# Kernel tuning notes

Hardware: AMD Instinct MI355X
Metric: run time of the kernel (lower is better)

Reference implementation:

```python
import jax, jax.numpy as jnp
import numpy as np

B, T, FEAT, IN = 32, 96, 2048, 4096  # batch, frames, feature_len, inshape (cat mode)


def setup_inputs() -> dict:
    key = jax.random.key(0)
    ks = jax.random.split(key, 12)
    s = 1.0 / np.sqrt(FEAT)  # PyTorch LSTMCell/Linear init scale ~ U(-1/sqrt(hidden), ...)
    f32 = jnp.float32
    return {
        "feature": jax.random.normal(ks[0], (B, T, IN), f32),
        "gumbel_u": jax.random.uniform(ks[1], (T - 1, B, 2), f32),
        "W_ih": jax.random.normal(ks[2], (4 * FEAT, IN), f32) * s,
        "b_ih": jax.random.normal(ks[3], (4 * FEAT,), f32) * s,
        "W_hh": jax.random.normal(ks[4], (4 * FEAT, FEAT), f32) * s,
        "b_hh": jax.random.normal(ks[5], (4 * FEAT,), f32) * s,
        "W_pred": jax.random.normal(ks[6], (2, FEAT), f32) * s,
        "b_pred": jax.random.normal(ks[7], (2,), f32) * s,
        "W_util": jax.random.normal(ks[8], (1, FEAT), f32) * s,
        "b_util": jax.random.normal(ks[9], (1,), f32) * s,
        "W_use": jax.random.normal(ks[10], (2, FEAT), f32) * s,
        "b_use": jax.random.normal(ks[11], (2,), f32) * s,
    }


def reference(feature, gumbel_u, W_ih, b_ih, W_hh, b_hh,
              W_pred, b_pred, W_util, b_util, W_use, b_use):
    tau = 1.0
    eps = 1e-10
    x = jnp.transpose(feature, (1, 0, 2))          # [T, B, IN]
    gnoise = -jnp.log(-jnp.log(gumbel_u + eps) + eps)  # Gumbel(0,1), [T-1, B, 2]

    def lstm_cell(x_t, h, c):
        gates = x_t @ W_ih.T + b_ih + h @ W_hh.T + b_hh  # [B, 4F]
        i, f, g, o = jnp.split(gates, 4, axis=-1)        # PyTorch gate order i,f,g,o
        c2 = jax.nn.sigmoid(f) * c + jax.nn.sigmoid(i) * jnp.tanh(g)
        h2 = jax.nn.sigmoid(o) * jnp.tanh(c2)
        return h2, c2

    def heads(h):
        return h @ W_pred.T + b_pred, h @ W_util.T + b_util

    h0 = jnp.zeros((x.shape[1], FEAT), x.dtype)
    h, c = lstm_cell(x[0], h0, h0)                   # step 0: no gating
    pred0, util0 = heads(h)

    def step(carry, inp):
        h_prev, c_prev = carry
        x_t, g_t = inp
        h_new, c2 = lstm_cell(x_t, h_prev, c_prev)
        logits = h_new @ W_use.T + b_use             # [B, 2]
        use = jax.nn.softmax((logits + g_t) / tau, axis=-1)  # soft gumbel-softmax
        # bmm(stack([h_prev, h_new], -1), use) == convex mix of the two states
        h2 = h_prev * use[:, :1] + h_new * use[:, 1:2]
        pred, util = heads(h2)
        return (h2, c2), (pred, util)

    _, (preds, utils) = jax.lax.scan(step, (h, c), (x[1:], gnoise))
    pred = jnp.concatenate([pred0[None], preds], axis=0)   # [T, B, 2]
    util = jnp.concatenate([util0[None], utils], axis=0)   # [T, B, 1]
    return pred, util
```

## Files before the change

kernel.cpp:

```cpp
#include <hip/hip_runtime.h>
#include <cstdint>
#include <cstddef>

#define TT 96
#define BB 32
#define FEATD 2048
#define IND 4096
#define NG 8192
#define MROWS 3072

typedef _Float16 half8 __attribute__((ext_vector_type(8)));
typedef _Float16 half4 __attribute__((ext_vector_type(4)));
typedef _Float16 half2v __attribute__((ext_vector_type(2)));
typedef float f32x4 __attribute__((ext_vector_type(4)));

#define WS_FEAT16 0u
#define WS_HBUF   0u
#define WS_WIH16  25165824u
#define WS_WHH16  92274688u
#define WS_PRE16  125829120u
#define WS_GAB    176160768u
#define WS_HD     176185344u
#define WS_BAR    176222208u

#define NWG 256
#define BAR_WORDS 8192

__global__ void __launch_bounds__(256) k_convert(
    const float* __restrict__ feat, const float* __restrict__ wih,
    const float* __restrict__ whh,
    _Float16* __restrict__ feat16, _Float16* __restrict__ wih16,
    _Float16* __restrict__ whh16, unsigned* __restrict__ flags)
{
  size_t id = (size_t)blockIdx.x * blockDim.x + threadIdx.x;
  size_t stride = (size_t)gridDim.x * blockDim.x;
  for (size_t i = id; i < (size_t)MROWS * IND / 4; i += stride) {
    f32x4 v = ((const f32x4*)feat)[i];
    half4 h = { (_Float16)v[0], (_Float16)v[1], (_Float16)v[2], (_Float16)v[3] };
    ((half4*)feat16)[i] = h;
  }
  for (size_t i = id; i < (size_t)NG * IND / 4; i += stride) {
    f32x4 v = ((const f32x4*)wih)[i];
    half4 h = { (_Float16)v[0], (_Float16)v[1], (_Float16)v[2], (_Float16)v[3] };
    ((half4*)wih16)[i] = h;
  }
  for (size_t i = id; i < (size_t)NG * FEATD / 4; i += stride) {
    f32x4 v = ((const f32x4*)whh)[i];
    half4 h = { (_Float16)v[0], (_Float16)v[1], (_Float16)v[2], (_Float16)v[3] };
    ((half4*)whh16)[i] = h;
  }
  for (size_t i = id; i < BAR_WORDS; i += stride) flags[i] = 0u;
}

__device__ __forceinline__ void gload16(const _Float16* g, _Float16* l) {
  __builtin_amdgcn_global_load_lds(
      (const __attribute__((address_space(1))) void*)g,
      (__attribute__((address_space(3))) void*)l, 16, 0, 0);
}

__global__ void __launch_bounds__(256, 1) k_gemm(
    const _Float16* __restrict__ A,
    const _Float16* __restrict__ Bw,
    const float* __restrict__ bih, const float* __restrict__ bhh,
    _Float16* __restrict__ C)
{
  __shared__ __align__(16) _Float16 As[128 * 32];
  __shared__ __align__(16) _Float16 Bs[128 * 32];
  const int tid = threadIdx.x;
  const int lane = tid & 63;
  const int wave = tid >> 6;
  const int wm = wave >> 1, wn = wave & 1;
  const int mbase = blockIdx.y * 128;
  const int nbase = blockIdx.x * 128;

  f32x4 acc[4][4] = {};
  const int r0 = lane >> 2;
  const int kc = (lane & 3) * 8;
  const int rr = lane & 15;
  const int ko = (lane >> 4) * 8;

  for (int k0 = 0; k0 < IND; k0 += 32) {
    for (int i = 0; i < 2; ++i) {
      int seg = wave * 2 + i;
      int row = seg * 16 + r0;
      gload16(A + (size_t)(mbase + row) * IND + k0 + kc, As + seg * 512);
      gload16(Bw + (size_t)(nbase + row) * IND + k0 + kc, Bs + seg * 512);
    }
    __syncthreads();
    half8 af[4], bf[4];
    for (int f = 0; f < 4; ++f) {
      af[f] = *(const half8*)(As + (wm * 64 + f * 16 + rr) * 32 + ko);
      bf[f] = *(const half8*)(Bs + (wn * 64 + f * 16 + rr) * 32 + ko);
    }
    for (int fm = 0; fm < 4; ++fm)
      for (int fn = 0; fn < 4; ++fn)
        acc[fm][fn] = __builtin_amdgcn_mfma_f32_16x16x32_f16(af[fm], bf[fn], acc[fm][fn], 0, 0, 0);
    __syncthreads();
  }
  for (int fn = 0; fn < 4; ++fn) {
    int n = nbase + wn * 64 + fn * 16 + (lane & 15);
    float bias = bih[n] + bhh[n];
    for (int fm = 0; fm < 4; ++fm) {
      int m0 = mbase + wm * 64 + fm * 16 + (lane >> 4) * 4;
      for (int r = 0; r < 4; ++r)
        C[(size_t)(m0 + r) * NG + n] = (_Float16)(acc[fm][fn][r] + bias);
    }
  }
}

#define LDS_WHH 0
#define LDS_RED 131072
#define RED_STRIDE_F 1152
#define LDS_TOTAL 149504

__device__ __forceinline__ float fast_sigmoid(float x) {
  return 1.f / (1.f + __expf(-x));
}
__device__ __forceinline__ float fast_tanh(float x) {
  return 1.f - 2.f / (__expf(2.f * x) + 1.f);
}

__global__ void __launch_bounds__(512, 1) k_recur(
    const float* __restrict__ gumbel,
    const float* __restrict__ Wuse, const float* __restrict__ buse,
    const _Float16* __restrict__ whh16,
    const _Float16* __restrict__ pre16,
    _Float16* __restrict__ hbuf,
    float* __restrict__ gab,
    unsigned* __restrict__ flags)
{
  extern __shared__ __align__(16) char smem[];
  const int tid = threadIdx.x;
  const int wg = blockIdx.x;
  const int wave = tid >> 6, lane = tid & 63;
  float* RED = (float*)(smem + LDS_RED);

  {
    int c = tid >> 4;
    int grow = (c >> 3) * FEATD + wg * 8 + (c & 7);
    const _Float16* src = whh16 + (size_t)grow * FEATD;
    char* dst = smem + LDS_WHH + c * 4096;
    int x = c & 7;
    for (int i = 0; i < 16; ++i) {
      int g = (tid & 15) + i * 16;
      *(half8*)(dst + ((g ^ x) << 4)) = *(const half8*)(src + g * 8);
    }
  }

  const int rr = lane & 15;
  const int lk = (lane >> 4) * 8;
  half8 uq0[8], uq1[8];
#pragma unroll
  for (int s = 0; s < 8; ++s) {
    int kk = wave * 256 + s * 32 + lk;
#pragma unroll
    for (int e = 0; e < 8; ++e) {
      uq0[s][e] = (_Float16)Wuse[kk + e];
      uq1[s][e] = (_Float16)Wuse[FEATD + kk + e];
    }
  }

  const int b_ = tid >> 3, fi_ = tid & 7;
  const float bq0 = buse[0], bq1 = buse[1];

  float G0 = 0.f, G1 = 0.f, G2 = 0.f, G3 = 0.f, cc = 0.f;
  const _Float16* prbase = pre16 + ((size_t)b_ * TT) * NG + wg * 8 + fi_;
  _Float16 pf0 = 0, pf1 = 0, pf2 = 0, pf3 = 0;
  _Float16 pn0 = 0, pn1 = 0, pn2 = 0, pn3 = 0;
  float gmc0 = 0.f, gmc1 = 0.f, gmn0 = 0.f, gmn1 = 0.f;
  if (tid < 256) {
    pf0 = prbase[0]; pf1 = prbase[FEATD]; pf2 = prbase[2 * FEATD]; pf3 = prbase[3 * FEATD];
  }
  __syncthreads();

  for (int t = 0; t < TT; ++t) {
    if (tid < 256 && t + 1 < TT) {
      const _Float16* p = prbase + (size_t)(t + 1) * NG;
      pn0 = p[0]; pn1 = p[FEATD]; pn2 = p[2 * FEATD]; pn3 = p[3 * FEATD];
      gmn0 = gumbel[(size_t)t * 64 + b_ * 2 + 0];
      gmn1 = gumbel[(size_t)t * 64 + b_ * 2 + 1];
    }
    if (tid < 256) {
      float ig = fast_sigmoid((float)pf0 + G0);
      float fg = fast_sigmoid((float)pf1 + G1);
      float gg = fast_tanh((float)pf2 + G2);
      float og = fast_sigmoid((float)pf3 + G3);
      cc = fg * cc + ig * gg;
      float hn = og * fast_tanh(cc);
      float hn_o = __shfl_xor(hn, 1);
      if ((fi_ & 1) == 0) {
        union { _Float16 h[2]; unsigned u; } pk;
        pk.h[0] = (_Float16)hn; pk.h[1] = (_Float16)hn_o;
        unsigned* dst = (unsigned*)(hbuf + (size_t)t * (BB * FEATD) + b_ * FEATD + wg * 8 + fi_);
        __hip_atomic_store(dst, pk.u, __ATOMIC_RELAXED, __HIP_MEMORY_SCOPE_AGENT);
      }
    }
    __syncthreads();
    const unsigned tgt = (unsigned)(t + 1);
    if (tid == 0)
      __hip_atomic_store(&flags[wg * 16], tgt, __ATOMIC_RELAXED, __HIP_MEMORY_SCOPE_AGENT);
    if (wg == 0) {
      if (wave == 0) {
        for (;;) {
          bool ok = true;
#pragma unroll
          for (int j = 0; j < 4; ++j) {
            unsigned v = __hip_atomic_load(&flags[(lane * 4 + j) * 16],
                                           __ATOMIC_RELAXED, __HIP_MEMORY_SCOPE_AGENT);
            ok &= (v >= tgt);
          }
          if (__all(ok)) break;
          __builtin_amdgcn_s_sleep(1);
        }
#pragma unroll
        for (int j = 0; j < 4; ++j)
          __hip_atomic_store(&flags[4096 + (lane * 4 + j) * 16], tgt,
                             __ATOMIC_RELAXED, __HIP_MEMORY_SCOPE_AGENT);
      }
    } else {
      if (tid == 0) {
        while (__hip_atomic_load(&flags[4096 + wg * 16],
                                 __ATOMIC_RELAXED, __HIP_MEMORY_SCOPE_AGENT) < tgt)
          __builtin_amdgcn_s_sleep(1);
      }
    }
    __syncthreads();

    const _Float16* hb = hbuf + (size_t)t * (BB * FEATD);
    f32x4 acc[2][2] = {};
    float q0a = 0.f, q1a = 0.f, q0b = 0.f, q1b = 0.f;
    {
      const int c0 = rr, c1 = 16 + rr;
      const char* wsl = smem + LDS_WHH;
#pragma unroll
      for (int s = 0; s < 8; ++s) {
        int kk = wave * 256 + s * 32 + lk;
        half8 a0 = *(const half8*)(hb + rr * FEATD + kk);
        half8 a1 = *(const half8*)(hb + (16 + rr) * FEATD + kk);
        int g = kk >> 3;
        half8 b0 = *(const half8*)(wsl + c0 * 4096 + ((g ^ (c0 & 7)) << 4));
        half8 b1 = *(const half8*)(wsl + c1 * 4096 + ((g ^ (c1 & 7)) << 4));
        acc[0][0] = __builtin_amdgcn_mfma_f32_16x16x32_f16(a0, b0, acc[0][0], 0, 0, 0);
        acc[0][1] = __builtin_amdgcn_mfma_f32_16x16x32_f16(a0, b1, acc[0][1], 0, 0, 0);
        acc[1][0] = __builtin_amdgcn_mfma_f32_16x16x32_f16(a1, b0, acc[1][0], 0, 0, 0);
        acc[1][1] = __builtin_amdgcn_mfma_f32_16x16x32_f16(a1, b1, acc[1][1], 0, 0, 0);
        const half2v* a0p = (const half2v*)&a0;
        const half2v* a1p = (const half2v*)&a1;
        const half2v* u0p = (const half2v*)&uq0[s];
        const half2v* u1p = (const half2v*)&uq1[s];
#pragma unroll
        for (int e = 0; e < 4; ++e) {
          q0a = __builtin_amdgcn_fdot2(a0p[e], u0p[e], q0a, false);
          q1a = __builtin_amdgcn_fdot2(a0p[e], u1p[e], q1a, false);
          q0b = __builtin_amdgcn_fdot2(a1p[e], u0p[e], q0b, false);
          q1b = __builtin_amdgcn_fdot2(a1p[e], u1p[e], q1b, false);
        }
      }
    }
    q0a += __shfl_xor(q0a, 16); q0a += __shfl_xor(q0a, 32);
    q1a += __shfl_xor(q1a, 16); q1a += __shfl_xor(q1a, 32);
    q0b += __shfl_xor(q0b, 16); q0b += __shfl_xor(q0b, 32);
    q1b += __shfl_xor(q1b, 16); q1b += __shfl_xor(q1b, 32);
    if (lane < 16) {
      float* pads = RED + (wave & 3) * RED_STRIDE_F + 32 + (wave >> 2) * 2;
      pads[rr * 36 + 0] = q0a; pads[rr * 36 + 1] = q1a;
      pads[(16 + rr) * 36 + 0] = q0b; pads[(16 + rr) * 36 + 1] = q1b;
    }
    {
      const int bb0 = (lane >> 4) * 4;
      const int cc0 = lane & 15;
      if (wave >= 4) {
        float* s0 = RED + (wave - 4) * RED_STRIDE_F;
        for (int fm = 0; fm < 2; ++fm)
          for (int fn = 0; fn < 2; ++fn)
            *(f32x4*)(s0 + (fn * 16 + cc0) * 36 + fm * 16 + bb0) = acc[fm][fn];
      }
      __syncthreads();
      if (wave < 4) {
        float* s0 = RED + wave * RED_STRIDE_F;
        for (int fm = 0; fm < 2; ++fm)
          for (int fn = 0; fn < 2; ++fn) {
            acc[fm][fn] += *(f32x4*)(s0 + (fn * 16 + cc0) * 36 + fm * 16 + bb0);
            *(f32x4*)(s0 + (fn * 16 + cc0) * 36 + fm * 16 + bb0) = acc[fm][fn];
          }
      }
      __syncthreads();
    }
    if (tid < 256) {
      float ga = 0.f, gb = 1.f;
      if (t > 0) {
        float q0 = bq0, q1 = bq1;
#pragma unroll
        for (int s2 = 0; s2 < 4; ++s2) {
          const float* pp = RED + s2 * RED_STRIDE_F + b_ * 36 + 32;
          q0 += pp[0] + pp[2]; q1 += pp[1] + pp[3];
        }
        float n0 = -logf(-logf(gmc0 + 1e-10f) + 1e-10f);
        float n1 = -logf(-logf(gmc1 + 1e-10f) + 1e-10f);
        float l0 = q0 + n0;
        float l1 = q1 + n1;
        float mx = fmaxf(l0, l1);
        float e0 = __expf(l0 - mx), e1 = __expf(l1 - mx);
        float inv = 1.f / (e0 + e1);
        ga = e0 * inv; gb = e1 * inv;
        if (wg == 0 && fi_ == 0) {
          gab[(t * BB + b_) * 2 + 0] = ga;
          gab[(t * BB + b_) * 2 + 1] = gb;
        }
      }
      {
        const int base = fi_ * 36 + b_;
        float m0 = RED[base] + RED[RED_STRIDE_F + base] + RED[2 * RED_STRIDE_F + base] + RED[3 * RED_STRIDE_F + base];
        float m1 = RED[base + 8 * 36] + RED[RED_STRIDE_F + base + 8 * 36] + RED[2 * RED_STRIDE_F + base + 8 * 36] + RED[3 * RED_STRIDE_F + base + 8 * 36];
        float m2 = RED[base + 16 * 36] + RED[RED_STRIDE_F + base + 16 * 36] + RED[2 * RED_STRIDE_F + base + 16 * 36] + RED[3 * RED_STRIDE_F + base + 16 * 36];
        float m3 = RED[base + 24 * 36] + RED[RED_STRIDE_F + base + 24 * 36] + RED[2 * RED_STRIDE_F + base + 24 * 36] + RED[3 * RED_STRIDE_F + base + 24 * 36];
        G0 = ga * G0 + gb * m0;
        G1 = ga * G1 + gb * m1;
        G2 = ga * G2 + gb * m2;
        G3 = ga * G3 + gb * m3;
      }
      pf0 = pn0; pf1 = pn1; pf2 = pn2; pf3 = pn3;
      gmc0 = gmn0; gmc1 = gmn1;
    }
  }
}

__global__ void __launch_bounds__(256) k_heads(
    const _Float16* __restrict__ hbuf,
    const float* __restrict__ Wpred, const float* __restrict__ Wutil,
    float* __restrict__ hd)
{
  const int t = blockIdx.x;
  const int tid = threadIdx.x;
  const int b = tid >> 3, fi = tid & 7;
  const _Float16* h = hbuf + ((size_t)t * BB + b) * FEATD;
  float d0 = 0.f, d1 = 0.f, d2 = 0.f;
  for (int j = 0; j < 32; ++j) {
    int k = fi * 8 + j * 64;
    half8 v = *(const half8*)(h + k);
#pragma unroll
    for (int e = 0; e < 8; ++e) {
      float x = (float)v[e];
      d0 += x * Wpred[k + e];
      d1 += x * Wpred[FEATD + k + e];
      d2 += x * Wutil[k + e];
    }
  }
  for (int m = 1; m < 8; m <<= 1) {
    d0 += __shfl_xor(d0, m); d1 += __shfl_xor(d1, m); d2 += __shfl_xor(d2, m);
  }
  if (fi == 0) {
    float* o = hd + ((size_t)t * BB + b) * 3;
    o[0] = d0; o[1] = d1; o[2] = d2;
  }
}

__global__ void __launch_bounds__(64) k_scan(
    const float* __restrict__ hd,
    const float* __restrict__ gab,
    const float* __restrict__ bpred, const float* __restrict__ butil,
    float* __restrict__ out)
{
  const int b = threadIdx.x;
  if (b >= BB) return;
  const float bp0 = bpred[0], bp1 = bpred[1], bu0 = butil[0];
  float L0 = hd[b * 3 + 0], L1 = hd[b * 3 + 1], L2 = hd[b * 3 + 2];
  out[b * 2 + 0] = L0 + bp0;
  out[b * 2 + 1] = L1 + bp1;
  out[TT * BB * 2 + b] = L2 + bu0;
  for (int t = 1; t < TT; ++t) {
    float ga = gab[(t * BB + b) * 2 + 0];
    float gb = gab[(t * BB + b) * 2 + 1];
    const float* d = hd + ((size_t)t * BB + b) * 3;
    L0 = ga * L0 + gb * d[0];
    L1 = ga * L1 + gb * d[1];
    L2 = ga * L2 + gb * d[2];
    out[(t * BB + b) * 2 + 0] = L0 + bp0;
    out[(t * BB + b) * 2 + 1] = L1 + bp1;
    out[TT * BB * 2 + t * BB + b] = L2 + bu0;
  }
}

extern "C" void kernel_launch(void* const* d_in, const int* in_sizes, int n_in,
                              void* d_out, int out_size, void* d_ws, size_t ws_size,
                              hipStream_t stream) {
  const float* feat  = (const float*)d_in[0];
  const float* gumb  = (const float*)d_in[1];
  const float* Wih   = (const float*)d_in[2];
  const float* bih   = (const float*)d_in[3];
  const float* Whh   = (const float*)d_in[4];
  const float* bhh   = (const float*)d_in[5];
  const float* Wpred = (const float*)d_in[6];
  const float* bpred = (const float*)d_in[7];
  const float* Wutil = (const float*)d_in[8];
  const float* butil = (const float*)d_in[9];
  const float* Wuse  = (const float*)d_in[10];
  const float* buse  = (const float*)d_in[11];

  char* ws = (char*)d_ws;
  _Float16* feat16 = (_Float16*)(ws + WS_FEAT16);
  _Float16* hbufp  = (_Float16*)(ws + WS_HBUF);
  _Float16* wih16  = (_Float16*)(ws + WS_WIH16);
  _Float16* whh16  = (_Float16*)(ws + WS_WHH16);
  _Float16* pre16  = (_Float16*)(ws + WS_PRE16);
  float*    gabp   = (float*)(ws + WS_GAB);
  float*    hdp    = (float*)(ws + WS_HD);
  unsigned* flagp  = (unsigned*)(ws + WS_BAR);

  (void)in_sizes; (void)n_in; (void)out_size; (void)ws_size;

  hipFuncSetAttribute((const void*)k_recur,
                      hipFuncAttributeMaxDynamicSharedMemorySize, LDS_TOTAL);

  k_convert<<<2048, 256, 0, stream>>>(feat, Wih, Whh, feat16, wih16, whh16, flagp);
  dim3 g2(NG / 128, MROWS / 128);
  k_gemm<<<g2, 256, 0, stream>>>(feat16, wih16, bih, bhh, pre16);
  k_recur<<<NWG, 512, LDS_TOTAL, stream>>>(gumb, Wuse, buse, whh16, pre16,
                                           hbufp, gabp, flagp);
  k_heads<<<TT, 256, 0, stream>>>(hbufp, Wpred, Wutil, hdp);
  k_scan<<<1, 64, 0, stream>>>(hdp, gabp, bpred, butil, (float*)d_out);
}
```

Baseline: 1.044 ms.

## Split batch into two half-groups and ping-pong recurrence phases across grid barriers

The 32-batch recurrence is split into two independent 16-row halves (A and B) with separate flag sets and LDS reduction buffers. While one half waits on its grid-wide barrier, the other half's h·W_hh matmul and gate update run, so barrier latency overlaps with compute. This adds extra barriers, more per-step phases, and more complex flag and gumbel index bookkeeping that must stay correct.

```diff
diff --git a/kernel.cpp b/kernel.cpp
--- a/kernel.cpp
+++ b/kernel.cpp
@@ -24,7 +24,11 @@
 #define WS_BAR    176222208u
 
 #define NWG 256
-#define BAR_WORDS 8192
+#define BAR_WORDS 16384
+#define AR_A 0
+#define AR_B 4096
+#define RL_A 8192
+#define RL_B 12288
 
 __global__ void __launch_bounds__(256) k_convert(
     const float* __restrict__ feat, const float* __restrict__ wih,
@@ -109,15 +113,87 @@
 }
 
 #define LDS_WHH 0
-#define LDS_RED 131072
-#define RED_STRIDE_F 1152
-#define LDS_TOTAL 149504
+#define SLOT_F 640
+#define LDS_REDA 131072
+#define LDS_REDB 141312
+#define LDS_TOTAL 151552
 
 __device__ __forceinline__ float fast_sigmoid(float x) {
   return 1.f / (1.f + __expf(-x));
 }
 __device__ __forceinline__ float fast_tanh(float x) {
   return 1.f - 2.f / (__expf(2.f * x) + 1.f);
+}
+
+__device__ __forceinline__ void agg_release(unsigned* flags, int arBase, int rlBase,
+                                            unsigned tgt, int lane) {
+  for (;;) {
+    bool ok = true;
+#pragma unroll
+    for (int j = 0; j < 4; ++j) {
+      unsigned v = __hip_atomic_load(&flags[arBase + (lane * 4 + j) * 16],
+                                     __ATOMIC_RELAXED, __HIP_MEMORY_SCOPE_AGENT);
+      ok &= (v >= tgt);
+    }
+    if (__all(ok)) break;
+    __builtin_amdgcn_s_sleep(1);
+  }
+#pragma unroll
+  for (int j = 0; j < 4; ++j)
+    __hip_atomic_store(&flags[rlBase + (lane * 4 + j) * 16], tgt,
+                       __ATOMIC_RELAXED, __HIP_MEMORY_SCOPE_AGENT);
+}
+
+__device__ __forceinline__ void phase2(const _Float16* __restrict__ hbX,
+                                       const char* __restrict__ wsl,
+                                       float* __restrict__ REDX,
+                                       const half8* __restrict__ uq0,
+                                       const half8* __restrict__ uq1,
+                                       int wave, int lane, int rr, int lk) {
+  f32x4 acc0 = {}, acc1 = {};
+  float q0 = 0.f, q1 = 0.f;
+  const int c0 = rr, c1 = 16 + rr;
+#pragma unroll
+  for (int s = 0; s < 8; ++s) {
+    int kk = wave * 256 + s * 32 + lk;
+    half8 a0 = *(const half8*)(hbX + rr * FEATD + kk);
+    int g = kk >> 3;
+    half8 b0 = *(const half8*)(wsl + c0 * 4096 + ((g ^ (c0 & 7)) << 4));
+    half8 b1 = *(const half8*)(wsl + c1 * 4096 + ((g ^ (c1 & 7)) << 4));
+    acc0 = __builtin_amdgcn_mfma_f32_16x16x32_f16(a0, b0, acc0, 0, 0, 0);
+    acc1 = __builtin_amdgcn_mfma_f32_16x16x32_f16(a0, b1, acc1, 0, 0, 0);
+    const half2v* ap  = (const half2v*)&a0;
+    const half2v* u0p = (const half2v*)&uq0[s];
+    const half2v* u1p = (const half2v*)&uq1[s];
+#pragma unroll
+    for (int e = 0; e < 4; ++e) {
+      q0 = __builtin_amdgcn_fdot2(ap[e], u0p[e], q0, false);
+      q1 = __builtin_amdgcn_fdot2(ap[e], u1p[e], q1, false);
+    }
+  }
+  q0 += __shfl_xor(q0, 16); q0 += __shfl_xor(q0, 32);
+  q1 += __shfl_xor(q1, 16); q1 += __shfl_xor(q1, 32);
+  if (lane < 16) {
+    float* pads = REDX + (wave & 3) * SLOT_F + rr * 20 + 16 + (wave >> 2) * 2;
+    pads[0] = q0; pads[1] = q1;
+  }
+  const int bb0 = (lane >> 4) * 4;
+  const int cc0 = lane & 15;
+  if (wave >= 4) {
+    float* s0 = REDX + (wave - 4) * SLOT_F;
+    *(f32x4*)(s0 + cc0 * 20 + bb0) = acc0;
+    *(f32x4*)(s0 + (16 + cc0) * 20 + bb0) = acc1;
+  }
+  __syncthreads();
+  if (wave < 4) {
+    float* s0 = REDX + wave * SLOT_F;
+    f32x4 t0 = *(f32x4*)(s0 + cc0 * 20 + bb0);
+    f32x4 t1 = *(f32x4*)(s0 + (16 + cc0) * 20 + bb0);
+    t0 += acc0; t1 += acc1;
+    *(f32x4*)(s0 + cc0 * 20 + bb0) = t0;
+    *(f32x4*)(s0 + (16 + cc0) * 20 + bb0) = t1;
+  }
+  __syncthreads();
 }
 
 __global__ void __launch_bounds__(512, 1) k_recur(
@@ -133,7 +209,9 @@
   const int tid = threadIdx.x;
   const int wg = blockIdx.x;
   const int wave = tid >> 6, lane = tid & 63;
-  float* RED = (float*)(smem + LDS_RED);
+  float* REDA = (float*)(smem + LDS_REDA);
+  float* REDB = (float*)(smem + LDS_REDB);
+  const char* wsl = smem + LDS_WHH;
 
   {
     int c = tid >> 4;
@@ -160,27 +238,25 @@
     }
   }
 
-  const int b_ = tid >> 3, fi_ = tid & 7;
+  const bool isA = tid < 128;
+  const bool isB = (tid >= 128 && tid < 256);
+  const int bg = (tid & 127) >> 3;
+  const int fi_ = tid & 7;
+  const int bglob = (isB ? 16 : 0) + bg;
   const float bq0 = buse[0], bq1 = buse[1];
 
   float G0 = 0.f, G1 = 0.f, G2 = 0.f, G3 = 0.f, cc = 0.f;
-  const _Float16* prbase = pre16 + ((size_t)b_ * TT) * NG + wg * 8 + fi_;
+  const _Float16* prbase = pre16 + ((size_t)bglob * TT) * NG + wg * 8 + fi_;
   _Float16 pf0 = 0, pf1 = 0, pf2 = 0, pf3 = 0;
-  _Float16 pn0 = 0, pn1 = 0, pn2 = 0, pn3 = 0;
-  float gmc0 = 0.f, gmc1 = 0.f, gmn0 = 0.f, gmn1 = 0.f;
-  if (tid < 256) {
+  float gmc0 = 0.f, gmc1 = 0.f;
+  if (isA || isB) {
     pf0 = prbase[0]; pf1 = prbase[FEATD]; pf2 = prbase[2 * FEATD]; pf3 = prbase[3 * FEATD];
   }
   __syncthreads();
 
   for (int t = 0; t < TT; ++t) {
-    if (tid < 256 && t + 1 < TT) {
-      const _Float16* p = prbase + (size_t)(t + 1) * NG;
-      pn0 = p[0]; pn1 = p[FEATD]; pn2 = p[2 * FEATD]; pn3 = p[3 * FEATD];
-      gmn0 = gumbel[(size_t)t * 64 + b_ * 2 + 0];
-      gmn1 = gumbel[(size_t)t * 64 + b_ * 2 + 1];
-    }
-    if (tid < 256) {
+    const unsigned tgt = (unsigned)(t + 1);
+    if (isA) {
       float ig = fast_sigmoid((float)pf0 + G0);
       float fg = fast_sigmoid((float)pf1 + G1);
       float gg = fast_tanh((float)pf2 + G2);
@@ -191,136 +267,154 @@
       if ((fi_ & 1) == 0) {
         union { _Float16 h[2]; unsigned u; } pk;
         pk.h[0] = (_Float16)hn; pk.h[1] = (_Float16)hn_o;
-        unsigned* dst = (unsigned*)(hbuf + (size_t)t * (BB * FEATD) + b_ * FEATD + wg * 8 + fi_);
+        unsigned* dst = (unsigned*)(hbuf + (size_t)t * (BB * FEATD) + bglob * FEATD + wg * 8 + fi_);
         __hip_atomic_store(dst, pk.u, __ATOMIC_RELAXED, __HIP_MEMORY_SCOPE_AGENT);
       }
     }
     __syncthreads();
-    const unsigned tgt = (unsigned)(t + 1);
     if (tid == 0)
-      __hip_atomic_store(&flags[wg * 16], tgt, __ATOMIC_RELAXED, __HIP_MEMORY_SCOPE_AGENT);
-    if (wg == 0) {
-      if (wave == 0) {
-        for (;;) {
-          bool ok = true;
-#pragma unroll
-          for (int j = 0; j < 4; ++j) {
-            unsigned v = __hip_atomic_load(&flags[(lane * 4 + j) * 16],
-                                           __ATOMIC_RELAXED, __HIP_MEMORY_SCOPE_AGENT);
-            ok &= (v >= tgt);
+      __hip_atomic_store(&flags[AR_A + wg * 16], tgt, __ATOMIC_RELAXED, __HIP_MEMORY_SCOPE_AGENT);
+    if (isA && t + 1 < TT) {
+      const _Float16* p = prbase + (size_t)(t + 1) * NG;
+      pf0 = p[0]; pf1 = p[FEATD]; pf2 = p[2 * FEATD]; pf3 = p[3 * FEATD];
+    }
+
+    if (t > 0) {
+      if (tid == 0) {
+        while (__hip_atomic_load(&flags[RL_B + wg * 16], __ATOMIC_RELAXED, __HIP_MEMORY_SCOPE_AGENT) < (unsigned)t)
+          __builtin_amdgcn_s_sleep(1);
+      }
+      __syncthreads();
+      phase2(hbuf + (size_t)(t - 1) * (BB * FEATD) + 16 * FEATD, wsl, REDB, uq0, uq1, wave, lane, rr, lk);
+      if (wg == 0 && wave == 4) agg_release(flags, AR_A, RL_A, tgt, lane);
+      if (isB) {
+        float ga = 0.f, gb = 1.f;
+        if (t > 1) {
+          float q0 = bq0, q1 = bq1;
+#pragma unroll
+          for (int s2 = 0; s2 < 4; ++s2) {
+            const float* pp = REDB + s2 * SLOT_F + bg * 20 + 16;
+            q0 += pp[0] + pp[2]; q1 += pp[1] + pp[3];
           }
-          if (__all(ok)) break;
-          __builtin_amdgcn_s_sleep(1);
+          float n0 = -logf(-logf(gmc0 + 1e-10f) + 1e-10f);
+          float n1 = -logf(-logf(gmc1 + 1e-10f) + 1e-10f);
+          float l0 = q0 + n0, l1 = q1 + n1;
+          float mx = fmaxf(l0, l1);
+          float e0 = __expf(l0 - mx), e1 = __expf(l1 - mx);
+          float inv = 1.f / (e0 + e1);
+          ga = e0 * inv; gb = e1 * inv;
+          if (wg == 0 && fi_ == 0) {
+            gab[((t - 1) * BB + bglob) * 2 + 0] = ga;
+            gab[((t - 1) * BB + bglob) * 2 + 1] = gb;
+          }
         }
 #pragma unroll
-        for (int j = 0; j < 4; ++j)
-          __hip_atomic_store(&flags[4096 + (lane * 4 + j) * 16], tgt,
-                             __ATOMIC_RELAXED, __HIP_MEMORY_SCOPE_AGENT);
+        for (int j = 0; j < 4; ++j) {
+          int c = fi_ + 8 * j;
+          float m = REDB[c * 20 + bg] + REDB[SLOT_F + c * 20 + bg]
+                  + REDB[2 * SLOT_F + c * 20 + bg] + REDB[3 * SLOT_F + c * 20 + bg];
+          if (j == 0) G0 = ga * G0 + gb * m;
+          else if (j == 1) G1 = ga * G1 + gb * m;
+          else if (j == 2) G2 = ga * G2 + gb * m;
+          else G3 = ga * G3 + gb * m;
+        }
       }
     } else {
-      if (tid == 0) {
-        while (__hip_atomic_load(&flags[4096 + wg * 16],
-                                 __ATOMIC_RELAXED, __HIP_MEMORY_SCOPE_AGENT) < tgt)
-          __builtin_amdgcn_s_sleep(1);
+      if (wg == 0 && wave == 4) agg_release(flags, AR_A, RL_A, 1u, lane);
+    }
+
+    if (isB) {
+      float ig = fast_sigmoid((float)pf0 + G0);
+      float fg = fast_sigmoid((float)pf1 + G1);
+      float gg = fast_tanh((float)pf2 + G2);
+      float og = fast_sigmoid((float)pf3 + G3);
+      cc = fg * cc + ig * gg;
+      float hn = og * fast_tanh(cc);
+      float hn_o = __shfl_xor(hn, 1);
+      if ((fi_ & 1) == 0) {
+        union { _Float16 h[2]; unsigned u; } pk;
+        pk.h[0] = (_Float16)hn; pk.h[1] = (_Float16)hn_o;
+        unsigned* dst = (unsigned*)(hbuf + (size_t)t * (BB * FEATD) + bglob * FEATD + wg * 8 + fi_);
+        __hip_atomic_store(dst, pk.u, __ATOMIC_RELAXED, __HIP_MEMORY_SCOPE_AGENT);
+      }
+      if (t + 1 < TT) {
+        const _Float16* p = prbase + (size_t)(t + 1) * NG;
+        pf0 = p[0]; pf1 = p[FEATD]; pf2 = p[2 * FEATD]; pf3 = p[3 * FEATD];
+      }
+      if (t >= 1) {
+        gmc0 = gumbel[(size_t)(t - 1) * 64 + bglob * 2 + 0];
+        gmc1 = gumbel[(size_t)(t - 1) * 64 + bglob * 2 + 1];
       }
     }
     __syncthreads();
-
-    const _Float16* hb = hbuf + (size_t)t * (BB * FEATD);
-    f32x4 acc[2][2] = {};
-    float q0a = 0.f, q1a = 0.f, q0b = 0.f, q1b = 0.f;
-    {
-      const int c0 = rr, c1 = 16 + rr;
-      const char* wsl = smem + LDS_WHH;
-#pragma unroll
-      for (int s = 0; s < 8; ++s) {
-        int kk = wave * 256 + s * 32 + lk;
-        half8 a0 = *(const half8*)(hb + rr * FEATD + kk);
-        half8 a1 = *(const half8*)(hb + (16 + rr) * FEATD + kk);
-        int g = kk >> 3;
-        half8 b0 = *(const half8*)(wsl + c0 * 4096 + ((g ^ (c0 & 7)) << 4));
-        half8 b1 = *(const half8*)(wsl + c1 * 4096 + ((g ^ (c1 & 7)) << 4));
-        acc[0][0] = __builtin_amdgcn_mfma_f32_16x16x32_f16(a0, b0, acc[0][0], 0, 0, 0);
-        acc[0][1] = __builtin_amdgcn_mfma_f32_16x16x32_f16(a0, b1, acc[0][1], 0, 0, 0);
-        acc[1][0] = __builtin_amdgcn_mfma_f32_16x16x32_f16(a1, b0, acc[1][0], 0, 0, 0);
-        acc[1][1] = __builtin_amdgcn_mfma_f32_16x16x32_f16(a1, b1, acc[1][1], 0, 0, 0);
-        const half2v* a0p = (const half2v*)&a0;
-        const half2v* a1p = (const half2v*)&a1;
-        const half2v* u0p = (const half2v*)&uq0[s];
-        const half2v* u1p = (const half2v*)&uq1[s];
-#pragma unroll
-        for (int e = 0; e < 4; ++e) {
-          q0a = __builtin_amdgcn_fdot2(a0p[e], u0p[e], q0a, false);
-          q1a = __builtin_amdgcn_fdot2(a0p[e], u1p[e], q1a, false);
-          q0b = __builtin_amdgcn_fdot2(a1p[e], u0p[e], q0b, false);
-          q1b = __builtin_amdgcn_fdot2(a1p[e], u1p[e], q1b, false);
-        }
-      }
-    }
-    q0a += __shfl_xor(q0a, 16); q0a += __shfl_xor(q0a, 32);
-    q1a += __shfl_xor(q1a, 16); q1a += __shfl_xor(q1a, 32);
-    q0b += __shfl_xor(q0b, 16); q0b += __shfl_xor(q0b, 32);
-    q1b += __shfl_xor(q1b, 16); q1b += __shfl_xor(q1b, 32);
-    if (lane < 16) {
-      float* pads = RED + (wave & 3) * RED_STRIDE_F + 32 + (wave >> 2) * 2;
-      pads[rr * 36 + 0] = q0a; pads[rr * 36 + 1] = q1a;
-      pads[(16 + rr) * 36 + 0] = q0b; pads[(16 + rr) * 36 + 1] = q1b;
-    }
-    {
-      const int bb0 = (lane >> 4) * 4;
-      const int cc0 = lane & 15;
-      if (wave >= 4) {
-        float* s0 = RED + (wave - 4) * RED_STRIDE_F;
-        for (int fm = 0; fm < 2; ++fm)
-          for (int fn = 0; fn < 2; ++fn)
-            *(f32x4*)(s0 + (fn * 16 + cc0) * 36 + fm * 16 + bb0) = acc[fm][fn];
-      }
-      __syncthreads();
-      if (wave < 4) {
-        float* s0 = RED + wave * RED_STRIDE_F;
-        for (int fm = 0; fm < 2; ++fm)
-          for (int fn = 0; fn < 2; ++fn) {
-            acc[fm][fn] += *(f32x4*)(s0 + (fn * 16 + cc0) * 36 + fm * 16 + bb0);
-            *(f32x4*)(s0 + (fn * 16 + cc0) * 36 + fm * 16 + bb0) = acc[fm][fn];
-          }
-      }
-      __syncthreads();
-    }
-    if (tid < 256) {
+    if (tid == 0) {
+      __hip_atomic_store(&flags[AR_B + wg * 16], tgt, __ATOMIC_RELAXED, __HIP_MEMORY_SCOPE_AGENT);
+      while (__hip_atomic_load(&flags[RL_A + wg * 16], __ATOMIC_RELAXED, __HIP_MEMORY_SCOPE_AGENT) < tgt)
+        __builtin_amdgcn_s_sleep(1);
+    }
+    __syncthreads();
+    phase2(hbuf + (size_t)t * (BB * FEATD), wsl, REDA, uq0, uq1, wave, lane, rr, lk);
+    if (wg == 0 && wave == 4) agg_release(flags, AR_B, RL_B, tgt, lane);
+    if (isA) {
       float ga = 0.f, gb = 1.f;
       if (t > 0) {
         float q0 = bq0, q1 = bq1;
 #pragma unroll
         for (int s2 = 0; s2 < 4; ++s2) {
-          const float* pp = RED + s2 * RED_STRIDE_F + b_ * 36 + 32;
+          const float* pp = REDA + s2 * SLOT_F + bg * 20 + 16;
           q0 += pp[0] + pp[2]; q1 += pp[1] + pp[3];
         }
         float n0 = -logf(-logf(gmc0 + 1e-10f) + 1e-10f);
         float n1 = -logf(-logf(gmc1 + 1e-10f) + 1e-10f);
-        float l0 = q0 + n0;
-        float l1 = q1 + n1;
+        float l0 = q0 + n0, l1 = q1 + n1;
         float mx = fmaxf(l0, l1);
         float e0 = __expf(l0 - mx), e1 = __expf(l1 - mx);
         float inv = 1.f / (e0 + e1);
         ga = e0 * inv; gb = e1 * inv;
         if (wg == 0 && fi_ == 0) {
-          gab[(t * BB + b_) * 2 + 0] = ga;
-          gab[(t * BB + b_) * 2 + 1] = gb;
+          gab[(t * BB + bglob) * 2 + 0] = ga;
+          gab[(t * BB + bglob) * 2 + 1] = gb;
         }
       }
-      {
-        const int base = fi_ * 36 + b_;
-        float m0 = RED[base] + RED[RED_STRIDE_F + base] + RED[2 * RED_STRIDE_F + base] + RED[3 * RED_STRIDE_F + base];
-        float m1 = RED[base + 8 * 36] + RED[RED_STRIDE_F + base + 8 * 36] + RED[2 * RED_STRIDE_F + base + 8 * 36] + RED[3 * RED_STRIDE_F + base + 8 * 36];
-        float m2 = RED[base + 16 * 36] + RED[RED_STRIDE_F + base + 16 * 36] + RED[2 * RED_STRIDE_F + base + 16 * 36] + RED[3 * RED_STRIDE_F + base + 16 * 36];
-        float m3 = RED[base + 24 * 36] + RED[RED_STRIDE_F + base + 24 * 36] + RED[2 * RED_STRIDE_F + base + 24 * 36] + RED[3 * RED_STRIDE_F + base + 24 * 36];
-        G0 = ga * G0 + gb * m0;
-        G1 = ga * G1 + gb * m1;
-        G2 = ga * G2 + gb * m2;
-        G3 = ga * G3 + gb * m3;
-      }
-      pf0 = pn0; pf1 = pn1; pf2 = pn2; pf3 = pn3;
-      gmc0 = gmn0; gmc1 = gmn1;
+#pragma unroll
+      for (int j = 0; j < 4; ++j) {
+        int c = fi_ + 8 * j;
+        float m = REDA[c * 20 + bg] + REDA[SLOT_F + c * 20 + bg]
+                + REDA[2 * SLOT_F + c * 20 + bg] + REDA[3 * SLOT_F + c * 20 + bg];
+        if (j == 0) G0 = ga * G0 + gb * m;
+        else if (j == 1) G1 = ga * G1 + gb * m;
+        else if (j == 2) G2 = ga * G2 + gb * m;
+        else G3 = ga * G3 + gb * m;
+      }
+      if (t < TT - 1) {
+        gmc0 = gumbel[(size_t)t * 64 + bglob * 2 + 0];
+        gmc1 = gumbel[(size_t)t * 64 + bglob * 2 + 1];
+      }
+    }
+  }
+
+  if (tid == 0) {
+    while (__hip_atomic_load(&flags[RL_B + wg * 16], __ATOMIC_RELAXED, __HIP_MEMORY_SCOPE_AGENT) < (unsigned)TT)
+      __builtin_amdgcn_s_sleep(1);
+  }
+  __syncthreads();
+  phase2(hbuf + (size_t)(TT - 1) * (BB * FEATD) + 16 * FEATD, wsl, REDB, uq0, uq1, wave, lane, rr, lk);
+  if (isB) {
+    float q0 = bq0, q1 = bq1;
+#pragma unroll
+    for (int s2 = 0; s2 < 4; ++s2) {
+      const float* pp = REDB + s2 * SLOT_F + bg * 20 + 16;
+      q0 += pp[0] + pp[2]; q1 += pp[1] + pp[3];
+    }
+    float n0 = -logf(-logf(gmc0 + 1e-10f) + 1e-10f);
+    float n1 = -logf(-logf(gmc1 + 1e-10f) + 1e-10f);
+    float l0 = q0 + n0, l1 = q1 + n1;
+    float mx = fmaxf(l0, l1);
+    float e0 = __expf(l0 - mx), e1 = __expf(l1 - mx);
+    float inv = 1.f / (e0 + e1);
+    if (wg == 0 && fi_ == 0) {
+      gab[((TT - 1) * BB + bglob) * 2 + 0] = e0 * inv;
+      gab[((TT - 1) * BB + bglob) * 2 + 1] = e1 * inv;
     }
   }
 }
```

Result: slower. 1.094 ms (+4.7%).

## Rewrite input-projection GEMM with 256x128 tiles, double-buffered LDS and swizzling

Applied to the files above, without the earlier changes.

Replaces the simple 128x128 GEMM, which loads and syncs every 32-wide k step, with a 512-thread kernel. The new kernel computes 256x128 output tiles over 64-wide k steps and double-buffers the LDS loads so global-to-LDS copies overlap the MFMA work. It also XOR-swizzles the LDS layout to avoid bank conflicts, remaps block indices for L2 locality, and raises wave priority around the MFMA bursts. The aim is to cut load latency stalls and barrier overhead in the pre-gate GEMM, at the cost of more LDS per block and hand-written waitcnt/barrier ordering that must stay correct.

```diff
diff --git a/kernel.cpp b/kernel.cpp
--- a/kernel.cpp
+++ b/kernel.cpp
@@ -58,50 +58,123 @@
       (__attribute__((address_space(3))) void*)l, 16, 0, 0);
 }
 
-__global__ void __launch_bounds__(256, 1) k_gemm(
+#define GBUF 49152
+
+__global__ void __launch_bounds__(512, 1) k_gemm2(
     const _Float16* __restrict__ A,
     const _Float16* __restrict__ Bw,
     const float* __restrict__ bih, const float* __restrict__ bhh,
     _Float16* __restrict__ C)
 {
-  __shared__ __align__(16) _Float16 As[128 * 32];
-  __shared__ __align__(16) _Float16 Bs[128 * 32];
+  extern __shared__ __align__(16) char smem[];
   const int tid = threadIdx.x;
-  const int lane = tid & 63;
-  const int wave = tid >> 6;
-  const int wm = wave >> 1, wn = wave & 1;
-  const int mbase = blockIdx.y * 128;
-  const int nbase = blockIdx.x * 128;
+  const int l = tid & 63;
+  const int wv = tid >> 6;
+  const int wm = wv >> 1, wn = wv & 1;
+  const int rr = l & 15;
+
+  const int lin = blockIdx.x;
+  const int sw = (lin & 7) * 96 + (lin >> 3);
+  const int bx = sw & 63;
+  const int by = sw >> 6;
+  const int mbase = by * 256;
+  const int nbase = bx * 128;
+
+  const _Float16* Ablk = A + (size_t)mbase * IND;
+  const _Float16* Bblk = Bw + (size_t)nbase * IND;
+
+  const int gdat = (l & 3) ^ ((l >> 3) & 3);
+  const _Float16* gptr[3];
+  int ldsk0[3], ldsk1[3];
+#pragma unroll
+  for (int j = 0; j < 3; ++j) {
+    int c = wv * 3 + j;
+    bool isA = (c < 16);
+    int rowbase = isA ? c * 16 : (c - 16) * 16;
+    gptr[j] = (isA ? Ablk : Bblk) + (size_t)(rowbase + (l >> 2)) * IND + gdat * 8;
+    ldsk0[j] = (isA ? 0 : 32768) + rowbase * 64;
+    ldsk1[j] = (isA ? 16384 : 32768 + 8192) + rowbase * 64;
+  }
+
+  const int gpos = (l >> 4) ^ ((rr >> 1) & 3);
+  int offA[4], offB[4];
+#pragma unroll
+  for (int f = 0; f < 4; ++f) {
+    offA[f] = (wm * 64 + f * 16 + rr) * 64 + gpos * 16;
+    offB[f] = (wn * 64 + f * 16 + rr) * 64 + gpos * 16;
+  }
 
   f32x4 acc[4][4] = {};
-  const int r0 = lane >> 2;
-  const int kc = (lane & 3) * 8;
-  const int rr = lane & 15;
-  const int ko = (lane >> 4) * 8;
-
-  for (int k0 = 0; k0 < IND; k0 += 32) {
-    for (int i = 0; i < 2; ++i) {
-      int seg = wave * 2 + i;
-      int row = seg * 16 + r0;
-      gload16(A + (size_t)(mbase + row) * IND + k0 + kc, As + seg * 512);
-      gload16(Bw + (size_t)(nbase + row) * IND + k0 + kc, Bs + seg * 512);
-    }
-    __syncthreads();
-    half8 af[4], bf[4];
-    for (int f = 0; f < 4; ++f) {
-      af[f] = *(const half8*)(As + (wm * 64 + f * 16 + rr) * 32 + ko);
-      bf[f] = *(const half8*)(Bs + (wn * 64 + f * 16 + rr) * 32 + ko);
-    }
-    for (int fm = 0; fm < 4; ++fm)
-      for (int fn = 0; fn < 4; ++fn)
-        acc[fm][fn] = __builtin_amdgcn_mfma_f32_16x16x32_f16(af[fm], bf[fn], acc[fm][fn], 0, 0, 0);
-    __syncthreads();
-  }
+
+#pragma unroll
+  for (int j = 0; j < 3; ++j) gload16(gptr[j], (_Float16*)(smem + ldsk0[j]));
+#pragma unroll
+  for (int j = 0; j < 3; ++j) gload16(gptr[j] + 32, (_Float16*)(smem + ldsk1[j]));
+  asm volatile("s_waitcnt vmcnt(3)" ::: "memory");
+  asm volatile("s_barrier" ::: "memory");
+
+#pragma unroll 1
+  for (int tt = 0; tt < 64; ++tt) {
+    const char* cb = smem + (tt & 1) * GBUF;
+    char* nb = (char*)smem + ((tt & 1) ^ 1) * GBUF;
+    const int kt1 = (tt + 1) * 64;
+
+    {
+      half8 af[4], bf[4];
+#pragma unroll
+      for (int f = 0; f < 4; ++f) af[f] = *(const half8*)(cb + offA[f]);
+#pragma unroll
+      for (int f = 0; f < 4; ++f) bf[f] = *(const half8*)(cb + 32768 + offB[f]);
+      if (tt < 63) {
+#pragma unroll
+        for (int j = 0; j < 3; ++j)
+          gload16(gptr[j] + kt1, (_Float16*)(nb + ldsk0[j]));
+        asm volatile("s_waitcnt vmcnt(3)" ::: "memory");
+      } else {
+        asm volatile("s_waitcnt vmcnt(0)" ::: "memory");
+      }
+      asm volatile("s_barrier" ::: "memory");
+      __builtin_amdgcn_s_setprio(1);
+#pragma unroll
+      for (int fm = 0; fm < 4; ++fm)
+#pragma unroll
+        for (int fn = 0; fn < 4; ++fn)
+          acc[fm][fn] = __builtin_amdgcn_mfma_f32_16x16x32_f16(af[fm], bf[fn], acc[fm][fn], 0, 0, 0);
+      __builtin_amdgcn_s_setprio(0);
+      asm volatile("s_barrier" ::: "memory");
+    }
+    {
+      half8 af[4], bf[4];
+#pragma unroll
+      for (int f = 0; f < 4; ++f) af[f] = *(const half8*)(cb + 16384 + offA[f]);
+#pragma unroll
+      for (int f = 0; f < 4; ++f) bf[f] = *(const half8*)(cb + 32768 + 8192 + offB[f]);
+      if (tt < 63) {
+#pragma unroll
+        for (int j = 0; j < 3; ++j)
+          gload16(gptr[j] + kt1 + 32, (_Float16*)(nb + ldsk1[j]));
+        asm volatile("s_waitcnt vmcnt(3)" ::: "memory");
+      }
+      asm volatile("s_barrier" ::: "memory");
+      __builtin_amdgcn_s_setprio(1);
+#pragma unroll
+      for (int fm = 0; fm < 4; ++fm)
+#pragma unroll
+        for (int fn = 0; fn < 4; ++fn)
+          acc[fm][fn] = __builtin_amdgcn_mfma_f32_16x16x32_f16(af[fm], bf[fn], acc[fm][fn], 0, 0, 0);
+      __builtin_amdgcn_s_setprio(0);
+      asm volatile("s_barrier" ::: "memory");
+    }
+  }
+
+#pragma unroll
   for (int fn = 0; fn < 4; ++fn) {
-    int n = nbase + wn * 64 + fn * 16 + (lane & 15);
+    int n = nbase + wn * 64 + fn * 16 + (l & 15);
     float bias = bih[n] + bhh[n];
+#pragma unroll
     for (int fm = 0; fm < 4; ++fm) {
-      int m0 = mbase + wm * 64 + fm * 16 + (lane >> 4) * 4;
+      int m0 = mbase + wm * 64 + fm * 16 + (l >> 4) * 4;
+#pragma unroll
       for (int r = 0; r < 4; ++r)
         C[(size_t)(m0 + r) * NG + n] = (_Float16)(acc[fm][fn][r] + bias);
     }
@@ -409,12 +482,13 @@
 
   (void)in_sizes; (void)n_in; (void)out_size; (void)ws_size;
 
+  hipFuncSetAttribute((const void*)k_gemm2,
+                      hipFuncAttributeMaxDynamicSharedMemorySize, 2 * GBUF);
   hipFuncSetAttribute((const void*)k_recur,
                       hipFuncAttributeMaxDynamicSharedMemorySize, LDS_TOTAL);
 
   k_convert<<<2048, 256, 0, stream>>>(feat, Wih, Whh, feat16, wih16, whh16, flagp);
-  dim3 g2(NG / 128, MROWS / 128);
-  k_gemm<<<g2, 256, 0, stream>>>(feat16, wih16, bih, bhh, pre16);
+  k_gemm2<<<768, 512, 2 * GBUF, stream>>>(feat16, wih16, bih, bhh, pre16);
   k_recur<<<NWG, 512, LDS_TOTAL, stream>>>(gumb, Wuse, buse, whh16, pre16,
                                            hbufp, gabp, flagp);
   k_heads<<<TT, 256, 0, stream>>>(hbufp, Wpred, Wutil, hdp);
```

Result: faster. 1.015 ms (-2.8%).
